# Performance work log

Measured on AMD Instinct MI355X. Metric: run time of the kernel, lower is better.

## Reference

```python
import jax, jax.numpy as jnp
import numpy as np

T, N, L = 2048, 64, 300
V, E, H, KS, VS = 35, 256, 512, 128, 128


def _lstm_cell(x, h, c, Wih, Whh, bih, bhh):
    # PyTorch LSTMCell gate order: i, f, g, o
    gates = x @ Wih.T + bih + h @ Whh.T + bhh
    i, f, g, o = jnp.split(gates, 4, axis=-1)
    i = jax.nn.sigmoid(i)
    f = jax.nn.sigmoid(f)
    g = jnp.tanh(g)
    o = jax.nn.sigmoid(o)
    c = f * c + i * g
    h = o * jnp.tanh(c)
    return h, c


def setup_inputs() -> dict:
    key = jax.random.key(0)
    ks = jax.random.split(key, 16)
    s = 0.05
    emb_W = jax.random.normal(ks[0], (V, E), jnp.float32) * s
    emb_W = emb_W.at[0].set(0.0)  # padding_idx=0
    return {
        "key": jax.random.normal(ks[1], (T, N, KS), jnp.float32),
        "values": jax.random.normal(ks[2], (T, N, VS), jnp.float32),
        "x_lens": jax.random.randint(ks[3], (N,), 1, T, jnp.int32),
        "text": jax.random.randint(ks[4], (N, L), 0, V, jnp.int64),
        "emb_W": emb_W,
        "W_ih1": jax.random.normal(ks[5], (4 * H, E + VS), jnp.float32) * s,
        "W_hh1": jax.random.normal(ks[6], (4 * H, H), jnp.float32) * s,
        "b_ih1": jnp.zeros((4 * H,), jnp.float32),
        "b_hh1": jnp.zeros((4 * H,), jnp.float32),
        "W_ih2": jax.random.normal(ks[7], (4 * H, H), jnp.float32) * s,
        "W_hh2": jax.random.normal(ks[8], (4 * H, H), jnp.float32) * s,
        "b_ih2": jnp.zeros((4 * H,), jnp.float32),
        "b_hh2": jnp.zeros((4 * H,), jnp.float32),
        "W_ih3": jax.random.normal(ks[9], (4 * KS, H), jnp.float32) * s,
        "W_hh3": jax.random.normal(ks[10], (4 * KS, KS), jnp.float32) * s,
        "b_ih3": jnp.zeros((4 * KS,), jnp.float32),
        "b_hh3": jnp.zeros((4 * KS,), jnp.float32),
        "b_out": jnp.zeros((V,), jnp.float32),
    }


def reference(key, values, x_lens, text, emb_W,
              W_ih1, W_hh1, b_ih1, b_hh1,
              W_ih2, W_hh2, b_ih2, b_hh2,
              W_ih3, W_hh3, b_ih3, b_hh3, b_out):
    keyT = jnp.transpose(key, (1, 0, 2))     # (N, T, KS)
    valsT = jnp.transpose(values, (1, 0, 2))  # (N, T, VS)
    mask = jnp.arange(keyT.shape[1])[None, :] >= x_lens[:, None]  # (N, T)
    embeds = emb_W[text]                      # (N, L, E), teacher-forced (tf_rate=0)
    embeds = jnp.transpose(embeds, (1, 0, 2))  # (L, N, E)

    n = keyT.shape[0]
    carry0 = (jnp.zeros((n, H)), jnp.zeros((n, H)),
              jnp.zeros((n, H)), jnp.zeros((n, H)),
              jnp.zeros((n, KS)), jnp.zeros((n, KS)),
              jnp.zeros((n, VS)))

    def step(carry, char_embed):
        h1, c1, h2, c2, h3, c3, ctx = carry
        inp = jnp.concatenate([char_embed, ctx], axis=1)
        h1, c1 = _lstm_cell(inp, h1, c1, W_ih1, W_hh1, b_ih1, b_hh1)
        h2, c2 = _lstm_cell(h1, h2, c2, W_ih2, W_hh2, b_ih2, b_hh2)
        h3, c3 = _lstm_cell(h2, h3, c3, W_ih3, W_hh3, b_ih3, b_hh3)
        # attention: energy = bmm(key, query)
        energy = jnp.einsum('nte,ne->nt', keyT, h3)
        energy = jnp.where(mask, -1e9, energy)
        attn = jax.nn.softmax(energy, axis=1)
        ctx = jnp.einsum('nt,nte->ne', attn, valsT)
        logits = jnp.concatenate([h3, ctx], axis=1) @ emb_W.T + b_out
        return (h1, c1, h2, c2, h3, c3, ctx), (logits, attn)

    _, (preds, atts) = jax.lax.scan(step, carry0, embeds)
    predictions = jnp.transpose(preds, (1, 0, 2))  # (N, L, V)
    att = jnp.transpose(atts, (1, 0, 2))           # (N, L, T)
    return predictions, att
```

## Files before the change

kernel.cpp:

```cpp
#include <hip/hip_runtime.h>
#include <cstdint>
#include <cstddef>

#define T_ 2048
#define N_ 64
#define L_ 300
#define V_ 35
#define E_ 256
#define H_ 512
#define KS_ 128

typedef __attribute__((ext_vector_type(8))) short short8;
typedef __attribute__((ext_vector_type(4))) float float4v;

struct Params {
    const float *key, *values;
    const int *x_lens, *text;
    const float *emb_W;
    const float *W_ih1, *W_hh1, *b_ih1, *b_hh1;
    const float *W_ih2, *W_hh2, *b_ih2, *b_hh2;
    const float *W_ih3, *W_hh3, *b_ih3, *b_hh3;
    const float *b_out;
    unsigned short *W1P, *W2P, *W3P;
    float *embproj;
    float *b2, *b3;
    unsigned short *keyP;
    unsigned short *valP;
    unsigned int *bar;
    unsigned int *h1x0, *h1x1, *h2x0, *h2x1;
    float *h3xF;
    float *mqb, *sqb;
    float *ctxqb;
    float *out;
};

__device__ __forceinline__ float b2f(unsigned short u) {
    unsigned int i = ((unsigned int)u) << 16;
    float f; __builtin_memcpy(&f, &i, 4); return f;
}
__device__ __forceinline__ unsigned short f2b(float f) {
    unsigned int i; __builtin_memcpy(&i, &f, 4);
    i += 0x7FFFu + ((i >> 16) & 1u);
    return (unsigned short)(i >> 16);
}
__device__ __forceinline__ unsigned int packf2(float a, float b) {
    return (unsigned int)f2b(a) | ((unsigned int)f2b(b) << 16);
}
__device__ __forceinline__ float sigm(float x) { return 1.0f / (1.0f + __expf(-x)); }
__device__ __forceinline__ float tanh_(float x) {
    float e = __expf(2.0f * x);
    return 1.0f - 2.0f / (e + 1.0f);
}
__device__ __forceinline__ float wredsum(float v) {
#pragma unroll
    for (int o = 32; o > 0; o >>= 1) v += __shfl_down(v, o);
    return v;
}

__device__ __forceinline__ unsigned int cohLd(const unsigned int* p) {
    return __hip_atomic_load(p, __ATOMIC_RELAXED, __HIP_MEMORY_SCOPE_AGENT);
}
__device__ __forceinline__ void cohSt(unsigned int* p, unsigned int v) {
    __hip_atomic_store(p, v, __ATOMIC_RELAXED, __HIP_MEMORY_SCOPE_AGENT);
}
__device__ __forceinline__ float cohLdF(const float* p) {
    unsigned int u = __hip_atomic_load((const unsigned int*)p, __ATOMIC_RELAXED, __HIP_MEMORY_SCOPE_AGENT);
    float f; __builtin_memcpy(&f, &u, 4); return f;
}
__device__ __forceinline__ void cohStF(float* p, float v) {
    unsigned int u; __builtin_memcpy(&u, &v, 4);
    __hip_atomic_store((unsigned int*)p, u, __ATOMIC_RELAXED, __HIP_MEMORY_SCOPE_AGENT);
}

__device__ __forceinline__ void gbar_arrive(unsigned int* flags, int slot,
                                            unsigned int ep, int tid)
{
    asm volatile("s_waitcnt vmcnt(0)" ::: "memory");
    __syncthreads();
    if (tid == 0)
        __hip_atomic_store(flags + slot, ep, __ATOMIC_RELAXED, __HIP_MEMORY_SCOPE_AGENT);
}
__device__ __forceinline__ void gbar_wait(unsigned int* flags, unsigned int ep, int tid)
{
    if (tid < 64) {
        while (__hip_atomic_load(flags + tid, __ATOMIC_RELAXED, __HIP_MEMORY_SCOPE_AGENT) < ep)
            __builtin_amdgcn_s_sleep(1);
    }
    __syncthreads();
}

struct __align__(16) ShAB {
    unsigned short xs[16][1032];
    float gld[2][4][16][16];
};
struct __align__(16) ShC {
    unsigned int xk3u[320];
    float g3L[4][32];
};
struct __align__(16) ShD {
    float attl[512];
    float ctxp[32][129];
    float red[128];
    float lsum[V_][8];
};
union __align__(16) ShU { ShAB ab; ShC c; ShD d; };

template <int NKT>
__device__ __forceinline__ void gemm_ab(const unsigned short* xs,
                                        const unsigned short* wb,
                                        float (*gld)[4][16][16], int tid)
{
    const int lane = tid & 63, wv = tid >> 6;
    const int nt = wv & 1, ks = wv >> 1;
    constexpr int KTW = NKT / 4;
    float4v acc = {0.f, 0.f, 0.f, 0.f};
    const unsigned short* ar = xs + (lane & 15) * 1032 + ks * KTW * 32 + (lane >> 4) * 8;
    const unsigned short* wp = wb + ((size_t)(nt * NKT + ks * KTW)) * 512 + lane * 8;
#pragma unroll
    for (int k = 0; k < KTW; k++)
        acc = __builtin_amdgcn_mfma_f32_16x16x32_bf16(
            *(const short8*)(ar + k * 32), *(const short8*)(wp + (size_t)k * 512), acc, 0, 0, 0);
    const int q8 = lane >> 4, l15 = lane & 15;
#pragma unroll
    for (int r = 0; r < 4; r++) gld[nt][ks][l15][q8 * 4 + r] = acc[r];
}

__global__ __launch_bounds__(512) void decoder_main(Params p)
{
    __shared__ float c1L[128], c2L[128], c3L[32], h3sL[128];
    __shared__ float ctxf16[16][128];
    __shared__ float fL[16][4];
    __shared__ unsigned short h3bL[128];
    __shared__ ShU su;
    const int tid = threadIdx.x, wg = blockIdx.x;
    const int lane = tid & 63, wv = tid >> 6;
    const int mt = wg & 3, cp = wg >> 2;
    const int ownr = (wg >> 2) & 15, q = wg >> 6;
    const int n = mt * 16 + ownr;
    const int len = p.x_lens[n];
    const int rows_q = min(max(len - q * 512, 0), 512);
    float* const attnout = p.out + (size_t)N_ * L_ * V_ + (size_t)n * L_ * T_ + q * 512;
    unsigned int* const flags = p.bar + mt * 64;
    unsigned int ep = 0;

    if (tid < 128) { c1L[tid] = 0.f; c2L[tid] = 0.f; h3sL[tid] = 0.f; }
    if (tid < 32) c3L[tid] = 0.f;
    __syncthreads();

    const unsigned short* W1b = p.W1P + (size_t)cp * (2 * 20 * 512);
    const unsigned short* W2b = p.W2P + (size_t)cp * (2 * 32 * 512);
    const unsigned short* W3b = p.W3P + (size_t)(q * 8) * (20 * 512);

    unsigned int prefH1[10];
#pragma unroll
    for (int i = 0; i < 10; i++) prefH1[i] = 0u;

    auto combine = [&](int lp) {
        const int nr = tid >> 5, e0i = (tid & 31) * 4;
        float cq[4][4];
#pragma unroll
        for (int qq = 0; qq < 4; qq++) {
            const float* b = p.ctxqb + ((size_t)(mt * 16 + nr) * 4 + qq) * 128 + e0i;
#pragma unroll
            for (int j = 0; j < 4; j++) cq[qq][j] = cohLdF(b + j);
        }
        if (tid < 64)       su.d.red[tid] = cohLdF(p.mqb + mt * 64 + tid);
        else if (tid < 128) su.d.red[tid] = cohLdF(p.sqb + mt * 64 + (tid - 64));
        __syncthreads();
        if (tid < 16) {
            float m0 = su.d.red[tid * 4], m1 = su.d.red[tid * 4 + 1],
                  m2 = su.d.red[tid * 4 + 2], m3 = su.d.red[tid * 4 + 3];
            float M = fmaxf(fmaxf(m0, m1), fmaxf(m2, m3));
            float e0 = __expf(m0 - M), e1 = __expf(m1 - M),
                  e2 = __expf(m2 - M), e3 = __expf(m3 - M);
            float S = su.d.red[64 + tid * 4] * e0 + su.d.red[64 + tid * 4 + 1] * e1
                    + su.d.red[64 + tid * 4 + 2] * e2 + su.d.red[64 + tid * 4 + 3] * e3;
            float rS = 1.0f / S;
            fL[tid][0] = e0 * rS; fL[tid][1] = e1 * rS;
            fL[tid][2] = e2 * rS; fL[tid][3] = e3 * rS;
        }
        __syncthreads();
        {
            float fq = fL[ownr][q];
            if (tid < rows_q)
                __builtin_nontemporal_store(su.d.attl[tid] * fq,
                                            attnout + (size_t)lp * T_ + tid);
        }
        {
            float s0 = 0.f, s1 = 0.f, s2 = 0.f, s3 = 0.f;
#pragma unroll
            for (int qq = 0; qq < 4; qq++) {
                float f = fL[nr][qq];
                s0 += cq[qq][0] * f; s1 += cq[qq][1] * f;
                s2 += cq[qq][2] * f; s3 += cq[qq][3] * f;
            }
            ctxf16[nr][e0i] = s0; ctxf16[nr][e0i + 1] = s1;
            ctxf16[nr][e0i + 2] = s2; ctxf16[nr][e0i + 3] = s3;
        }
        __syncthreads();
        if (q == 0) {
            if (tid < V_ * 8) {
                const int v = tid >> 3, oc = tid & 7;
                const float* er = p.emb_W + (size_t)v * E_ + oc * 32;
                const float* src = (oc < 4) ? (h3sL + oc * 32) : (&ctxf16[ownr][0] + oc * 32 - 128);
                float s = 0.f;
#pragma unroll
                for (int j2 = 0; j2 < 32; j2++) s += src[j2] * er[j2];
                su.d.lsum[v][oc] = s;
            }
            __syncthreads();
            if (tid < V_) {
                float s = p.b_out[tid];
#pragma unroll
                for (int j2 = 0; j2 < 8; j2++) s += su.d.lsum[tid][j2];
                p.out[((size_t)n * L_ + lp) * V_ + tid] = s;
            }
        }
    };

    for (int l = 0; l < L_; ++l) {
        const unsigned int* h2prev = (l & 1) ? p.h2x1 : p.h2x0;
        unsigned int* h1cur        = (l & 1) ? p.h1x0 : p.h1x1;
        unsigned int* h2cur        = (l & 1) ? p.h2x0 : p.h2x1;

        gbar_wait(flags, ep, tid);
        float ebv[4];
        if (tid < 128) {
            const int m2e = mt * 16 + (tid & 15);
            const float* eb = p.embproj + (size_t)p.text[m2e * L_ + l] * 2048
                            + cp * 8 + (tid >> 4);
#pragma unroll
            for (int g = 0; g < 4; g++) ebv[g] = eb[g * 512];
        }
        if (l > 0) {
            combine(l - 1);
        } else {
            float* cf = &ctxf16[0][0];
            cf[tid * 4] = 0.f; cf[tid * 4 + 1] = 0.f;
            cf[tid * 4 + 2] = 0.f; cf[tid * 4 + 3] = 0.f;
        }
        __syncthreads();
        {
            unsigned int* xsu = (unsigned int*)&su.ab.xs[0][0];
#pragma unroll
            for (int i = 0; i < 10; i++) {
                int idx = tid + i * 512;
                int r = idx / 320, c = idx - r * 320;
                unsigned int u = (c < 64)
                    ? packf2(ctxf16[r][2 * c], ctxf16[r][2 * c + 1])
                    : prefH1[i];
                xsu[r * 516 + c] = u;
            }
        }
        __syncthreads();
        gemm_ab<20>(&su.ab.xs[0][0], W1b, su.ab.gld, tid);
        __syncthreads();
        if (tid < 128) {
            const int mm = tid & 15, j = tid >> 4;
            const int m2 = mt * 16 + mm;
            float gv[4];
#pragma unroll
            for (int g = 0; g < 4; g++) {
                int ntq = g >> 1, lq = (g & 1) * 8 + j;
                float s = 0.f;
#pragma unroll
                for (int k2 = 0; k2 < 4; k2++) s += su.ab.gld[ntq][k2][lq][mm];
                gv[g] = s + ebv[g];
            }
            float c = sigm(gv[1]) * c1L[tid] + sigm(gv[0]) * tanh_(gv[2]);
            c1L[tid] = c;
            unsigned int hb = (unsigned int)f2b(sigm(gv[3]) * tanh_(c));
            unsigned int ob = (unsigned int)__shfl_xor((int)hb, 16);
            if (!(j & 1)) cohSt(h1cur + m2 * 256 + cp * 4 + (j >> 1), hb | (ob << 16));
        }
        ++ep; gbar_arrive(flags, cp, ep, tid);

        unsigned int prefH2[16];
        if (tid >= 256) {
#pragma unroll
            for (int i = 0; i < 16; i++)
                prefH2[i] = cohLd(h2prev + (mt * 16 + i) * 256 + (tid - 256));
        }
        gbar_wait(flags, ep, tid);

        {
            unsigned int* xsu = (unsigned int*)&su.ab.xs[0][0];
#pragma unroll
            for (int i = 0; i < 16; i++) {
                unsigned int u = (tid < 256) ? cohLd(h1cur + (mt * 16 + i) * 256 + tid)
                                             : prefH2[i];
                xsu[i * 516 + tid] = u;
            }
            __syncthreads();
            gemm_ab<32>(&su.ab.xs[0][0], W2b, su.ab.gld, tid);
            __syncthreads();
            if (tid < 128) {
                const int mm = tid & 15, j = tid >> 4;
                const int m2 = mt * 16 + mm;
                float gv[4];
#pragma unroll
                for (int g = 0; g < 4; g++) {
                    int ntq = g >> 1, lq = (g & 1) * 8 + j;
                    float s = 0.f;
#pragma unroll
                    for (int k2 = 0; k2 < 4; k2++) s += su.ab.gld[ntq][k2][lq][mm];
                    gv[g] = s + p.b2[g * 512 + cp * 8 + j];
                }
                float c = sigm(gv[1]) * c2L[tid] + sigm(gv[0]) * tanh_(gv[2]);
                c2L[tid] = c;
                unsigned int hb = (unsigned int)f2b(sigm(gv[3]) * tanh_(c));
                unsigned int ob = (unsigned int)__shfl_xor((int)hb, 16);
                if (!(j & 1)) cohSt(h2cur + m2 * 256 + cp * 4 + (j >> 1), hb | (ob << 16));
            }
        }
        ++ep; gbar_arrive(flags, cp, ep, tid);
        gbar_wait(flags, ep, tid);

        {
            if (tid < 256) su.c.xk3u[tid] = cohLd(h2cur + n * 256 + tid);
            if (tid >= 256 && tid < 320) {
                int i2 = tid - 256;
                su.c.xk3u[256 + i2] = packf2(h3sL[2 * i2], h3sL[2 * i2 + 1]);
            }
            __syncthreads();
            const unsigned short* xb = (const unsigned short*)su.c.xk3u;
            const int q8 = lane >> 4;
            float4v acc = {0.f, 0.f, 0.f, 0.f};
            const unsigned short* ap = W3b + (size_t)wv * (20 * 512) + lane * 8;
#pragma unroll
            for (int kt = 0; kt < 20; kt++)
                acc = __builtin_amdgcn_mfma_f32_16x16x32_bf16(
                    *(const short8*)(ap + (size_t)kt * 512),
                    *(const short8*)(xb + kt * 32 + q8 * 8), acc, 0, 0, 0);
            if ((lane & 15) == 0) {
                const int g = wv >> 1, hl = (wv & 1) * 16 + q8 * 4;
                const float4v bb = *(const float4v*)(p.b3 + g * 128 + q * 32 + hl);
#pragma unroll
                for (int r = 0; r < 4; r++) su.c.g3L[g][hl + r] = acc[r] + bb[r];
            }
            __syncthreads();
            if (tid < 32) {
                float gi = sigm(su.c.g3L[0][tid]);
                float gf = sigm(su.c.g3L[1][tid]);
                float gg = tanh_(su.c.g3L[2][tid]);
                float go = sigm(su.c.g3L[3][tid]);
                float c = gf * c3L[tid] + gi * gg;
                c3L[tid] = c;
                cohStF(p.h3xF + n * 128 + q * 32 + tid, go * tanh_(c));
            }
        }
        ++ep; gbar_arrive(flags, cp, ep, tid);

        short8 kf[4][4];
        {
            const unsigned short* kpb = p.keyP + ((size_t)n * 128 + q * 32) * 2048;
#pragma unroll
            for (int i = 0; i < 4; i++) {
                int tl = wv * 4 + i;
                if (tl * 16 < rows_q) {
                    const unsigned short* ab2 = kpb + (size_t)tl * 2048 + lane * 8;
                    kf[i][0] = *(const short8*)(ab2);
                    kf[i][1] = *(const short8*)(ab2 + 512);
                    kf[i][2] = *(const short8*)(ab2 + 1024);
                    kf[i][3] = *(const short8*)(ab2 + 1536);
                }
            }
        }
        gbar_wait(flags, ep, tid);

        {
            if (tid < 128) {
                float h = cohLdF(p.h3xF + n * 128 + tid);
                h3sL[tid] = h;
                h3bL[tid] = f2b(h);
            }
            __syncthreads();
            const int q8 = lane >> 4, l15 = lane & 15;
            short8 bfr[4];
#pragma unroll
            for (int kq = 0; kq < 4; kq++)
                bfr[kq] = *(const short8*)(h3bL + kq * 32 + q8 * 8);
            float mloc = -1e30f;
#pragma unroll
            for (int i = 0; i < 4; i++) {
                int tl = wv * 4 + i;
                if (tl * 16 < rows_q) {
                    float4v acc = {0.f, 0.f, 0.f, 0.f};
                    acc = __builtin_amdgcn_mfma_f32_16x16x32_bf16(kf[i][0], bfr[0], acc, 0, 0, 0);
                    acc = __builtin_amdgcn_mfma_f32_16x16x32_bf16(kf[i][1], bfr[1], acc, 0, 0, 0);
                    acc = __builtin_amdgcn_mfma_f32_16x16x32_bf16(kf[i][2], bfr[2], acc, 0, 0, 0);
                    acc = __builtin_amdgcn_mfma_f32_16x16x32_bf16(kf[i][3], bfr[3], acc, 0, 0, 0);
                    int t0 = tl * 16 + q8 * 4;
#pragma unroll
                    for (int r = 0; r < 4; r++) {
                        float e = (t0 + r < rows_q) ? acc[r] : -1e30f;
                        acc[r] = e;
                        mloc = fmaxf(mloc, e);
                    }
                    if (l15 == 0) *(float4v*)(su.d.attl + t0) = acc;
                }
            }
            mloc = fmaxf(mloc, __shfl_xor(mloc, 16));
            mloc = fmaxf(mloc, __shfl_xor(mloc, 32));
            if (lane == 0) su.d.red[96 + wv] = mloc;
            __syncthreads();
            if (tid == 0) {
                float M2 = su.d.red[96];
                for (int i2 = 1; i2 < 8; i2++) M2 = fmaxf(M2, su.d.red[96 + i2]);
                su.d.red[112] = M2;
            }
            __syncthreads();
            const float M2 = su.d.red[112];
            float pv = (tid < rows_q) ? __expf(su.d.attl[tid] - M2) : 0.f;
            su.d.attl[tid] = pv;
            float ps = wredsum(pv);
            if (lane == 0) su.d.red[104 + wv] = ps;
            __syncthreads();
            if (tid == 0) {
                float s = 0.f;
                for (int i2 = 0; i2 < 8; i2++) s += su.d.red[104 + i2];
                cohStF(p.mqb + n * 4 + q, M2);
                cohStF(p.sqb + n * 4 + q, s);
            }
            __syncthreads();
            {
                const int tg = tid >> 4, e8 = tid & 15;
                float a8[8] = {0, 0, 0, 0, 0, 0, 0, 0};
                const unsigned short* vb = p.valP + ((size_t)n * 2048 + q * 512) * 128 + e8 * 8;
                int t = tg;
                for (; t + 96 < rows_q; t += 128) {
                    short8 v0 = *(const short8*)(vb + (size_t)t * 128);
                    short8 v1 = *(const short8*)(vb + (size_t)(t + 32) * 128);
                    short8 v2 = *(const short8*)(vb + (size_t)(t + 64) * 128);
                    short8 v3 = *(const short8*)(vb + (size_t)(t + 96) * 128);
                    float w0 = su.d.attl[t], w1 = su.d.attl[t + 32];
                    float w2 = su.d.attl[t + 64], w3 = su.d.attl[t + 96];
#pragma unroll
                    for (int j = 0; j < 8; j++)
                        a8[j] += w0 * b2f((unsigned short)v0[j]) + w1 * b2f((unsigned short)v1[j])
                               + w2 * b2f((unsigned short)v2[j]) + w3 * b2f((unsigned short)v3[j]);
                }
                for (; t < rows_q; t += 32) {
                    float w = su.d.attl[t];
                    short8 v8 = *(const short8*)(vb + (size_t)t * 128);
#pragma unroll
                    for (int j = 0; j < 8; j++) a8[j] += w * b2f((unsigned short)v8[j]);
                }
#pragma unroll
                for (int j = 0; j < 8; j++) su.d.ctxp[tg][e8 * 8 + j] = a8[j];
            }
            __syncthreads();
            if (tid < 128) {
                float s = 0.f;
#pragma unroll 8
                for (int g2 = 0; g2 < 32; g2++) s += su.d.ctxp[g2][tid];
                cohStF(p.ctxqb + ((size_t)n * 4 + q) * 128 + tid, s);
            }
        }
        ++ep; gbar_arrive(flags, cp, ep, tid);

        if (l + 1 < L_) {
#pragma unroll
            for (int i = 0; i < 10; i++) {
                int idx = tid + i * 512;
                int r = idx / 320, c = idx - r * 320;
                if (c >= 64)
                    prefH1[i] = cohLd(h1cur + (mt * 16 + r) * 256 + (c - 64));
            }
        }
    }
    gbar_wait(flags, ep, tid);
    combine(L_ - 1);
}

__global__ void setup_weights(Params p)
{
    size_t stride = (size_t)gridDim.x * blockDim.x;
    size_t i0 = (size_t)blockIdx.x * blockDim.x + threadIdx.x;
    for (size_t i = i0; i < (size_t)1310720; i += stride) {
        int e = (int)(i & 7), ln = (int)((i >> 3) & 63), blk = (int)(i >> 9);
        int kt = blk % 20, nt = (blk / 20) & 1, cpp = blk / 40;
        int l15 = ln & 15, q8 = ln >> 4;
        int col = (2 * nt + (l15 >> 3)) * 512 + cpp * 8 + (l15 & 7);
        int k = kt * 32 + q8 * 8 + e;
        float v = (k < 128) ? p.W_ih1[(size_t)col * 384 + 256 + k]
                            : p.W_hh1[(size_t)col * 512 + (k - 128)];
        p.W1P[i] = f2b(v);
    }
    for (size_t i = i0; i < (size_t)2097152; i += stride) {
        int e = (int)(i & 7), ln = (int)((i >> 3) & 63), blk = (int)(i >> 9);
        int kt = blk & 31, nt = (blk >> 5) & 1, cpp = blk >> 6;
        int l15 = ln & 15, q8 = ln >> 4;
        int col = (2 * nt + (l15 >> 3)) * 512 + cpp * 8 + (l15 & 7);
        int k = kt * 32 + q8 * 8 + e;
        float v = (k < 512) ? p.W_ih2[(size_t)col * 512 + k]
                            : p.W_hh2[(size_t)col * 512 + (k - 512)];
        p.W2P[i] = f2b(v);
    }
    for (size_t i = i0; i < (size_t)327680; i += stride) {
        int e = (int)(i & 7), ln = (int)((i >> 3) & 63), blk = (int)(i >> 9);
        int kt = blk % 20, tile = (blk / 20) & 7, qq = blk / 160;
        int l15 = ln & 15, q8 = ln >> 4;
        int col = (tile >> 1) * 128 + qq * 32 + (tile & 1) * 16 + l15;
        int k = kt * 32 + q8 * 8 + e;
        float v = (k < 512) ? p.W_ih3[(size_t)col * 512 + k]
                            : p.W_hh3[(size_t)col * 128 + (k - 512)];
        p.W3P[i] = f2b(v);
    }
    for (size_t i = i0; i < 2048; i += stride) p.b2[i] = p.b_ih2[i] + p.b_hh2[i];
    for (size_t i = i0; i < 512; i += stride) p.b3[i] = p.b_ih3[i] + p.b_hh3[i];
}

__global__ void setup_embproj(Params p)
{
    int idx = blockIdx.x * blockDim.x + threadIdx.x;
    if (idx >= V_ * 2048) return;
    int c = idx >> 11, j = idx & 2047;
    float s = p.b_ih1[j] + p.b_hh1[j];
    const float* er = p.emb_W + (size_t)c * E_;
    const float* wr = p.W_ih1 + (size_t)j * 384;
    for (int k = 0; k < 256; k++) s += er[k] * wr[k];
    p.embproj[idx] = s;
}

__global__ void setup_kv(Params p)
{
    size_t stride = (size_t)gridDim.x * blockDim.x;
    const size_t total = (size_t)T_ * N_ * KS_;
    for (size_t idx = (size_t)blockIdx.x * blockDim.x + threadIdx.x; idx < total; idx += stride) {
        int t = (int)(idx >> 13);
        int rem = (int)(idx & 8191);
        int n = rem >> 7, k = rem & 127;
        p.valP[((size_t)n * 2048 + t) * 128 + k] = f2b(p.values[idx]);
        size_t dst = (((size_t)n * 128 + (t >> 4)) * 4 + (k >> 5)) * 512
                   + ((((k >> 3) & 3) * 16 + (t & 15)) * 8) + (k & 7);
        p.keyP[dst] = f2b(p.key[idx]);
    }
}

extern "C" void kernel_launch(void* const* d_in, const int* in_sizes, int n_in,
                              void* d_out, int out_size, void* d_ws, size_t ws_size,
                              hipStream_t stream)
{
    (void)in_sizes; (void)n_in; (void)out_size; (void)ws_size;
    Params p;
    p.key    = (const float*)d_in[0];
    p.values = (const float*)d_in[1];
    p.x_lens = (const int*)d_in[2];
    p.text   = (const int*)d_in[3];
    p.emb_W  = (const float*)d_in[4];
    p.W_ih1  = (const float*)d_in[5];
    p.W_hh1  = (const float*)d_in[6];
    p.b_ih1  = (const float*)d_in[7];
    p.b_hh1  = (const float*)d_in[8];
    p.W_ih2  = (const float*)d_in[9];
    p.W_hh2  = (const float*)d_in[10];
    p.b_ih2  = (const float*)d_in[11];
    p.b_hh2  = (const float*)d_in[12];
    p.W_ih3  = (const float*)d_in[13];
    p.W_hh3  = (const float*)d_in[14];
    p.b_ih3  = (const float*)d_in[15];
    p.b_hh3  = (const float*)d_in[16];
    p.b_out  = (const float*)d_in[17];
    p.out    = (float*)d_out;

    char* w = (char*)d_ws;
    auto alloc = [&](size_t bytes) -> char* {
        char* r = w;
        w += (bytes + 255) & ~(size_t)255;
        return r;
    };
    p.W1P     = (unsigned short*)alloc((size_t)1310720 * 2);
    p.W2P     = (unsigned short*)alloc((size_t)2097152 * 2);
    p.W3P     = (unsigned short*)alloc((size_t)327680 * 2);
    p.embproj = (float*)alloc((size_t)V_ * 2048 * 4);
    p.b2      = (float*)alloc(2048 * 4);
    p.b3      = (float*)alloc(512 * 4);
    p.keyP    = (unsigned short*)alloc((size_t)16777216 * 2);
    p.valP    = (unsigned short*)alloc((size_t)16777216 * 2);
    char* zstart = w;
    p.bar   = (unsigned int*)alloc(4 * 64 * 4);
    p.h1x0  = (unsigned int*)alloc((size_t)N_ * 256 * 4);
    p.h1x1  = (unsigned int*)alloc((size_t)N_ * 256 * 4);
    p.h2x0  = (unsigned int*)alloc((size_t)N_ * 256 * 4);
    p.h2x1  = (unsigned int*)alloc((size_t)N_ * 256 * 4);
    p.h3xF  = (float*)alloc((size_t)N_ * 128 * 4);
    p.mqb   = (float*)alloc((size_t)N_ * 4 * 4);
    p.sqb   = (float*)alloc((size_t)N_ * 4 * 4);
    p.ctxqb = (float*)alloc((size_t)N_ * 4 * 128 * 4);
    size_t zbytes = (size_t)(w - zstart);

    hipMemsetAsync(zstart, 0, zbytes, stream);
    hipMemsetAsync((char*)d_out + (size_t)N_ * L_ * V_ * 4, 0,
                   (size_t)N_ * L_ * T_ * 4, stream);

    setup_weights<<<dim3(256), dim3(256), 0, stream>>>(p);
    setup_embproj<<<dim3(280), dim3(256), 0, stream>>>(p);
    setup_kv<<<dim3(2048), dim3(256), 0, stream>>>(p);

    void* args[] = { (void*)&p };
    hipLaunchCooperativeKernel((void*)decoder_main, dim3(256), dim3(512), args, 0, stream);
}
```

Measured before the change: 13.10 ms.

## Cache LSTM weights in LDS, interleave attention time tiles, streamline barrier wait

Each workgroup now copies its W1/W2 bf16 weight slices into shared memory once and runs the per-step GEMMs from LDS instead of global memory. Blocks are remapped to new (mt, cp) assignments. Attention time tiles are interleaved across the four quarter blocks so that padded-length work is spread evenly rather than piled onto the low quarters. The barrier wait now polls from every wave without a trailing __syncthreads, some redundant syncs are removed, and key/value streams use nontemporal loads. This costs about 104KB more LDS per block, which limits occupancy, and the barrier and sync removals carry ordering risk.

```diff
diff --git a/kernel.cpp b/kernel.cpp
--- a/kernel.cpp
+++ b/kernel.cpp
@@ -80,13 +80,10 @@
     if (tid == 0)
         __hip_atomic_store(flags + slot, ep, __ATOMIC_RELAXED, __HIP_MEMORY_SCOPE_AGENT);
 }
-__device__ __forceinline__ void gbar_wait(unsigned int* flags, unsigned int ep, int tid)
-{
-    if (tid < 64) {
-        while (__hip_atomic_load(flags + tid, __ATOMIC_RELAXED, __HIP_MEMORY_SCOPE_AGENT) < ep)
-            __builtin_amdgcn_s_sleep(1);
-    }
-    __syncthreads();
+__device__ __forceinline__ void gbar_wait(unsigned int* flags, unsigned int ep, int lane)
+{
+    while (__hip_atomic_load(flags + lane, __ATOMIC_RELAXED, __HIP_MEMORY_SCOPE_AGENT) < ep)
+        __builtin_amdgcn_s_sleep(1);
 }
 
 struct __align__(16) ShAB {
@@ -127,6 +124,8 @@
 
 __global__ __launch_bounds__(512) void decoder_main(Params p)
 {
+    __shared__ __align__(16) unsigned short W1L[20480];
+    __shared__ __align__(16) unsigned short W2L[32768];
     __shared__ float c1L[128], c2L[128], c3L[32], h3sL[128];
     __shared__ float ctxf16[16][128];
     __shared__ float fL[16][4];
@@ -134,21 +133,31 @@
     __shared__ ShU su;
     const int tid = threadIdx.x, wg = blockIdx.x;
     const int lane = tid & 63, wv = tid >> 6;
-    const int mt = wg & 3, cp = wg >> 2;
-    const int ownr = (wg >> 2) & 15, q = wg >> 6;
+    const int xid = wg & 7, jid = wg >> 3;
+    const int cp = (xid << 3) | (jid & 7);
+    const int mt = (jid >> 3) & 3;
+    const int ownr = cp & 15, q = cp >> 4;
     const int n = mt * 16 + ownr;
     const int len = p.x_lens[n];
-    const int rows_q = min(max(len - q * 512, 0), 512);
-    float* const attnout = p.out + (size_t)N_ * L_ * V_ + (size_t)n * L_ * T_ + q * 512;
+    const int kmax = (len > 16 * q) ? min(32, (len - 16 * q + 63) >> 6) : 0;
+    const int RQ = kmax << 4;
+    const int tglT = 64 * (tid >> 4) + 16 * q + (tid & 15);
+    float* const attnout = p.out + (size_t)N_ * L_ * V_ + (size_t)n * L_ * T_;
     unsigned int* const flags = p.bar + mt * 64;
     unsigned int ep = 0;
 
+    {
+        const short8* W1g = (const short8*)(p.W1P + (size_t)cp * (2 * 20 * 512));
+        const short8* W2g = (const short8*)(p.W2P + (size_t)cp * (2 * 32 * 512));
+#pragma unroll
+        for (int i = 0; i < 5; i++) ((short8*)W1L)[tid + i * 512] = W1g[tid + i * 512];
+#pragma unroll
+        for (int i = 0; i < 8; i++) ((short8*)W2L)[tid + i * 512] = W2g[tid + i * 512];
+    }
     if (tid < 128) { c1L[tid] = 0.f; c2L[tid] = 0.f; h3sL[tid] = 0.f; }
     if (tid < 32) c3L[tid] = 0.f;
     __syncthreads();
 
-    const unsigned short* W1b = p.W1P + (size_t)cp * (2 * 20 * 512);
-    const unsigned short* W2b = p.W2P + (size_t)cp * (2 * 32 * 512);
     const unsigned short* W3b = p.W3P + (size_t)(q * 8) * (20 * 512);
 
     unsigned int prefH1[10];
@@ -182,9 +191,9 @@
         __syncthreads();
         {
             float fq = fL[ownr][q];
-            if (tid < rows_q)
+            if (tglT < len)
                 __builtin_nontemporal_store(su.d.attl[tid] * fq,
-                                            attnout + (size_t)lp * T_ + tid);
+                                            attnout + (size_t)lp * T_ + tglT);
         }
         {
             float s0 = 0.f, s1 = 0.f, s2 = 0.f, s3 = 0.f;
@@ -223,8 +232,8 @@
         unsigned int* h1cur        = (l & 1) ? p.h1x0 : p.h1x1;
         unsigned int* h2cur        = (l & 1) ? p.h2x0 : p.h2x1;
 
-        gbar_wait(flags, ep, tid);
-        float ebv[4];
+        gbar_wait(flags, ep, lane);
+        float ebv[4] = {0.f, 0.f, 0.f, 0.f};
         if (tid < 128) {
             const int m2e = mt * 16 + (tid & 15);
             const float* eb = p.embproj + (size_t)p.text[m2e * L_ + l] * 2048
@@ -253,15 +262,15 @@
             }
         }
         __syncthreads();
-        gemm_ab<20>(&su.ab.xs[0][0], W1b, su.ab.gld, tid);
+        gemm_ab<20>(&su.ab.xs[0][0], W1L, su.ab.gld, tid);
         __syncthreads();
         if (tid < 128) {
-            const int mm = tid & 15, j = tid >> 4;
+            const int mm = tid & 15, jj = tid >> 4;
             const int m2 = mt * 16 + mm;
             float gv[4];
 #pragma unroll
             for (int g = 0; g < 4; g++) {
-                int ntq = g >> 1, lq = (g & 1) * 8 + j;
+                int ntq = g >> 1, lq = (g & 1) * 8 + jj;
                 float s = 0.f;
 #pragma unroll
                 for (int k2 = 0; k2 < 4; k2++) s += su.ab.gld[ntq][k2][lq][mm];
@@ -271,7 +280,7 @@
             c1L[tid] = c;
             unsigned int hb = (unsigned int)f2b(sigm(gv[3]) * tanh_(c));
             unsigned int ob = (unsigned int)__shfl_xor((int)hb, 16);
-            if (!(j & 1)) cohSt(h1cur + m2 * 256 + cp * 4 + (j >> 1), hb | (ob << 16));
+            if (!(jj & 1)) cohSt(h1cur + m2 * 256 + cp * 4 + (jj >> 1), hb | (ob << 16));
         }
         ++ep; gbar_arrive(flags, cp, ep, tid);
 
@@ -281,7 +290,7 @@
             for (int i = 0; i < 16; i++)
                 prefH2[i] = cohLd(h2prev + (mt * 16 + i) * 256 + (tid - 256));
         }
-        gbar_wait(flags, ep, tid);
+        gbar_wait(flags, ep, lane);
 
         {
             unsigned int* xsu = (unsigned int*)&su.ab.xs[0][0];
@@ -292,29 +301,29 @@
                 xsu[i * 516 + tid] = u;
             }
             __syncthreads();
-            gemm_ab<32>(&su.ab.xs[0][0], W2b, su.ab.gld, tid);
+            gemm_ab<32>(&su.ab.xs[0][0], W2L, su.ab.gld, tid);
             __syncthreads();
             if (tid < 128) {
-                const int mm = tid & 15, j = tid >> 4;
+                const int mm = tid & 15, jj = tid >> 4;
                 const int m2 = mt * 16 + mm;
                 float gv[4];
 #pragma unroll
                 for (int g = 0; g < 4; g++) {
-                    int ntq = g >> 1, lq = (g & 1) * 8 + j;
+                    int ntq = g >> 1, lq = (g & 1) * 8 + jj;
                     float s = 0.f;
 #pragma unroll
                     for (int k2 = 0; k2 < 4; k2++) s += su.ab.gld[ntq][k2][lq][mm];
-                    gv[g] = s + p.b2[g * 512 + cp * 8 + j];
+                    gv[g] = s + p.b2[g * 512 + cp * 8 + jj];
                 }
                 float c = sigm(gv[1]) * c2L[tid] + sigm(gv[0]) * tanh_(gv[2]);
                 c2L[tid] = c;
                 unsigned int hb = (unsigned int)f2b(sigm(gv[3]) * tanh_(c));
                 unsigned int ob = (unsigned int)__shfl_xor((int)hb, 16);
-                if (!(j & 1)) cohSt(h2cur + m2 * 256 + cp * 4 + (j >> 1), hb | (ob << 16));
+                if (!(jj & 1)) cohSt(h2cur + m2 * 256 + cp * 4 + (jj >> 1), hb | (ob << 16));
             }
         }
         ++ep; gbar_arrive(flags, cp, ep, tid);
-        gbar_wait(flags, ep, tid);
+        gbar_wait(flags, ep, lane);
 
         {
             if (tid < 256) su.c.xk3u[tid] = cohLd(h2cur + n * 256 + tid);
@@ -353,20 +362,20 @@
 
         short8 kf[4][4];
         {
-            const unsigned short* kpb = p.keyP + ((size_t)n * 128 + q * 32) * 2048;
+            const unsigned short* kpb = p.keyP + (size_t)n * (128 * 2048);
 #pragma unroll
             for (int i = 0; i < 4; i++) {
-                int tl = wv * 4 + i;
-                if (tl * 16 < rows_q) {
-                    const unsigned short* ab2 = kpb + (size_t)tl * 2048 + lane * 8;
-                    kf[i][0] = *(const short8*)(ab2);
-                    kf[i][1] = *(const short8*)(ab2 + 512);
-                    kf[i][2] = *(const short8*)(ab2 + 1024);
-                    kf[i][3] = *(const short8*)(ab2 + 1536);
+                int g = 4 * (wv * 4 + i) + q;
+                if (g * 16 < len) {
+                    const unsigned short* ab2 = kpb + (size_t)g * 2048 + lane * 8;
+                    kf[i][0] = __builtin_nontemporal_load((const short8*)(ab2));
+                    kf[i][1] = __builtin_nontemporal_load((const short8*)(ab2 + 512));
+                    kf[i][2] = __builtin_nontemporal_load((const short8*)(ab2 + 1024));
+                    kf[i][3] = __builtin_nontemporal_load((const short8*)(ab2 + 1536));
                 }
             }
         }
-        gbar_wait(flags, ep, tid);
+        gbar_wait(flags, ep, lane);
 
         {
             if (tid < 128) {
@@ -383,35 +392,35 @@
             float mloc = -1e30f;
 #pragma unroll
             for (int i = 0; i < 4; i++) {
-                int tl = wv * 4 + i;
-                if (tl * 16 < rows_q) {
+                int kloc = wv * 4 + i;
+                int g = 4 * kloc + q;
+                if (g * 16 < len) {
                     float4v acc = {0.f, 0.f, 0.f, 0.f};
                     acc = __builtin_amdgcn_mfma_f32_16x16x32_bf16(kf[i][0], bfr[0], acc, 0, 0, 0);
                     acc = __builtin_amdgcn_mfma_f32_16x16x32_bf16(kf[i][1], bfr[1], acc, 0, 0, 0);
                     acc = __builtin_amdgcn_mfma_f32_16x16x32_bf16(kf[i][2], bfr[2], acc, 0, 0, 0);
                     acc = __builtin_amdgcn_mfma_f32_16x16x32_bf16(kf[i][3], bfr[3], acc, 0, 0, 0);
-                    int t0 = tl * 16 + q8 * 4;
+                    int rbase = g * 16 + q8 * 4;
 #pragma unroll
                     for (int r = 0; r < 4; r++) {
-                        float e = (t0 + r < rows_q) ? acc[r] : -1e30f;
+                        float e = (rbase + r < len) ? acc[r] : -1e30f;
                         acc[r] = e;
                         mloc = fmaxf(mloc, e);
                     }
-                    if (l15 == 0) *(float4v*)(su.d.attl + t0) = acc;
+                    if (l15 == 0) *(float4v*)(su.d.attl + kloc * 16 + q8 * 4) = acc;
+                } else if (l15 == 0) {
+                    float4v z = {0.f, 0.f, 0.f, 0.f};
+                    *(float4v*)(su.d.attl + kloc * 16 + q8 * 4) = z;
                 }
             }
             mloc = fmaxf(mloc, __shfl_xor(mloc, 16));
             mloc = fmaxf(mloc, __shfl_xor(mloc, 32));
             if (lane == 0) su.d.red[96 + wv] = mloc;
             __syncthreads();
-            if (tid == 0) {
-                float M2 = su.d.red[96];
-                for (int i2 = 1; i2 < 8; i2++) M2 = fmaxf(M2, su.d.red[96 + i2]);
-                su.d.red[112] = M2;
-            }
-            __syncthreads();
-            const float M2 = su.d.red[112];
-            float pv = (tid < rows_q) ? __expf(su.d.attl[tid] - M2) : 0.f;
+            float M2 = su.d.red[96];
+#pragma unroll
+            for (int i2 = 1; i2 < 8; i2++) M2 = fmaxf(M2, su.d.red[96 + i2]);
+            float pv = (tglT < len) ? __expf(su.d.attl[tid] - M2) : 0.f;
             su.d.attl[tid] = pv;
             float ps = wredsum(pv);
             if (lane == 0) su.d.red[104 + wv] = ps;
@@ -422,27 +431,29 @@
                 cohStF(p.mqb + n * 4 + q, M2);
                 cohStF(p.sqb + n * 4 + q, s);
             }
-            __syncthreads();
             {
                 const int tg = tid >> 4, e8 = tid & 15;
                 float a8[8] = {0, 0, 0, 0, 0, 0, 0, 0};
-                const unsigned short* vb = p.valP + ((size_t)n * 2048 + q * 512) * 128 + e8 * 8;
-                int t = tg;
-                for (; t + 96 < rows_q; t += 128) {
-                    short8 v0 = *(const short8*)(vb + (size_t)t * 128);
-                    short8 v1 = *(const short8*)(vb + (size_t)(t + 32) * 128);
-                    short8 v2 = *(const short8*)(vb + (size_t)(t + 64) * 128);
-                    short8 v3 = *(const short8*)(vb + (size_t)(t + 96) * 128);
-                    float w0 = su.d.attl[t], w1 = su.d.attl[t + 32];
-                    float w2 = su.d.attl[t + 64], w3 = su.d.attl[t + 96];
+                const unsigned short* vb = p.valP
+                    + ((size_t)n * 2048 + 64 * (tg >> 4) + (tg & 15) + 16 * q) * 128 + e8 * 8;
+                const int smax = (RQ > tg) ? ((RQ - tg + 31) >> 5) : 0;
+                int s = 0;
+                for (; s + 3 < smax; s += 4) {
+                    const unsigned short* vp = vb + (size_t)s * 16384;
+                    short8 v0 = __builtin_nontemporal_load((const short8*)(vp));
+                    short8 v1 = __builtin_nontemporal_load((const short8*)(vp + 16384));
+                    short8 v2 = __builtin_nontemporal_load((const short8*)(vp + 32768));
+                    short8 v3 = __builtin_nontemporal_load((const short8*)(vp + 49152));
+                    float w0 = su.d.attl[tg + 32 * s],       w1 = su.d.attl[tg + 32 * (s + 1)];
+                    float w2 = su.d.attl[tg + 32 * (s + 2)], w3 = su.d.attl[tg + 32 * (s + 3)];
 #pragma unroll
                     for (int j = 0; j < 8; j++)
                         a8[j] += w0 * b2f((unsigned short)v0[j]) + w1 * b2f((unsigned short)v1[j])
                                + w2 * b2f((unsigned short)v2[j]) + w3 * b2f((unsigned short)v3[j]);
                 }
-                for (; t < rows_q; t += 32) {
-                    float w = su.d.attl[t];
-                    short8 v8 = *(const short8*)(vb + (size_t)t * 128);
+                for (; s < smax; s++) {
+                    float w = su.d.attl[tg + 32 * s];
+                    short8 v8 = __builtin_nontemporal_load((const short8*)(vb + (size_t)s * 16384));
 #pragma unroll
                     for (int j = 0; j < 8; j++) a8[j] += w * b2f((unsigned short)v8[j]);
                 }
@@ -469,7 +480,7 @@
             }
         }
     }
-    gbar_wait(flags, ep, tid);
+    gbar_wait(flags, ep, lane);
     combine(L_ - 1);
 }
 
```

After: 11.10 ms. -15.2%, faster.
